# Optimization experiments

Measured on AMD Instinct MI355X. Metric: run time of the kernel, lower is better.

The kernel has to match this reference:

```python
import jax, jax.numpy as jnp
import numpy as np

N_HEADS = 8
N_GROUPS = 32
EPS = 1e-6


def setup_inputs() -> dict:
    key = jax.random.key(0)
    ks = jax.random.split(key, 8)
    b, c, n, K = 2, 512, 1024, 64
    x = jax.random.normal(ks[0], (b, c, n), dtype=jnp.float32)
    valid_mask = jax.random.randint(ks[1], (n, K), 0, 2, dtype=jnp.int32)
    # ensure every query attends to at least one key (avoids all--inf softmax rows)
    valid_mask = valid_mask.at[:, 0].set(1)
    attend_idx = jax.random.randint(ks[2], (n, K), 0, n, dtype=jnp.int64)
    scale = 0.03
    return {
        "x": x,
        "valid_mask": valid_mask,
        "attend_idx": attend_idx,
        "gn_gamma": jnp.ones((c,), jnp.float32),
        "gn_beta": jnp.zeros((c,), jnp.float32),
        "wq": jax.random.normal(ks[3], (c, c), jnp.float32) * scale,
        "bq": jnp.zeros((c,), jnp.float32),
        "wk": jax.random.normal(ks[4], (c, c), jnp.float32) * scale,
        "bk": jnp.zeros((c,), jnp.float32),
        "wv": jax.random.normal(ks[5], (c, c), jnp.float32) * scale,
        "bv": jnp.zeros((c,), jnp.float32),
        "wo": jax.random.normal(ks[6], (c, c), jnp.float32) * scale,
        "bo": jnp.zeros((c,), jnp.float32),
    }


def _group_norm(x, gamma, beta):
    b, c, n = x.shape
    xr = x.reshape(b, N_GROUPS, c // N_GROUPS, n)
    mu = xr.mean(axis=(2, 3), keepdims=True)
    var = xr.var(axis=(2, 3), keepdims=True)
    h = ((xr - mu) * jax.lax.rsqrt(var + EPS)).reshape(b, c, n)
    return h * gamma[None, :, None] + beta[None, :, None]


def reference(x, valid_mask, attend_idx, gn_gamma, gn_beta,
              wq, bq, wk, bk, wv, bv, wo, bo):
    b, c, n = x.shape
    H = N_HEADS
    dh = c // H
    h = _group_norm(x, gn_gamma, gn_beta)
    # 1x1 Conv1d == per-node linear projection
    proj = lambda w, bias: jnp.einsum('oc,bcn->bon', w, h) + bias[None, :, None]
    q = proj(wq, bq).reshape(b, H, dh, n)
    k = proj(wk, bk).reshape(b, H, dh, n)
    v = proj(wv, bv).reshape(b, H, dh, n)
    # gather attendable keys/values per query: [b, H, nq, K, dh]
    kT = jnp.transpose(k, (0, 1, 3, 2))  # [b, H, n, dh]
    vT = jnp.transpose(v, (0, 1, 3, 2))
    keys = jnp.take(kT, attend_idx, axis=2)
    vals = jnp.take(vT, attend_idx, axis=2)
    # NOTE: sparse_forward uses beta=1 (no 1/sqrt(dh) scaling)
    w = jnp.einsum('bhqkc,bhcq->bhqk', keys, q)
    w = jnp.where(valid_mask[None, None] == 0, -jnp.inf, w)
    w = jax.nn.softmax(w, axis=-1)
    o = jnp.einsum('bhqk,bhqkc->bhqc', w, vals)  # [b, H, n, dh]
    # permute(0,3,1,2).reshape(b,c,n): channel layout is (dh, H)
    o = jnp.transpose(o, (0, 3, 1, 2)).reshape(b, c, n)
    out = x + jnp.einsum('oc,bcn->bon', wo, o) + bo[None, :, None]
    return out
```

## Files before the change

### kernel.cpp

```cpp
#include <hip/hip_runtime.h>
#include <hip/hip_bf16.h>

#define B_   2
#define C_   512
#define N_   1024
#define KK_  64
#define H_   8
#define DH_  64
#define NG_  32
#define MQKV 1536

typedef __attribute__((ext_vector_type(8))) short short8;
typedef __attribute__((ext_vector_type(4))) float f32x4;

__device__ __forceinline__ float ldf(const void* p, size_t i, int isbf) {
  return isbf ? __bfloat162float(((const __hip_bfloat16*)p)[i])
              : ((const float*)p)[i];
}
__device__ __forceinline__ unsigned short f2bfu(float f) {
  __hip_bfloat16 h = __float2bfloat16(f);
  unsigned short u; __builtin_memcpy(&u, &h, 2); return u;
}
__device__ __forceinline__ float bfu2f(unsigned short u) {
  return __uint_as_float(((unsigned)u) << 16);
}
__device__ __forceinline__ int detect_bf(const void* gamma) {
  return ((const unsigned*)gamma)[0] == 0x3F803F80u;
}
__device__ __forceinline__ uint4 ld8_bf(const void* w, size_t off, int isbf) {
  if (isbf) return *(const uint4*)((const unsigned short*)w + off);
  float4 a = *(const float4*)((const float*)w + off);
  float4 b = *(const float4*)((const float*)w + off + 4);
  uint4 u;
  u.x = (unsigned)f2bfu(a.x) | ((unsigned)f2bfu(a.y) << 16);
  u.y = (unsigned)f2bfu(a.z) | ((unsigned)f2bfu(a.w) << 16);
  u.z = (unsigned)f2bfu(b.x) | ((unsigned)f2bfu(b.y) << 16);
  u.w = (unsigned)f2bfu(b.z) | ((unsigned)f2bfu(b.w) << 16);
  return u;
}

__global__ __launch_bounds__(256) void conv_k(
    const void* x, const void* wq, const void* wk, const void* wv,
    const void* gamma, unsigned short* __restrict__ wqkvS,
    float2* __restrict__ part) {
  const int isbf = detect_bf(gamma);
  const int tid = threadIdx.x;
  const int idx = blockIdx.x * 256 + tid;
  {
    int m = idx >> 9, c = idx & 511;
    const void* src = (m < 512) ? wq : (m < 1024 ? wk : wv);
    wqkvS[idx] = f2bfu(ldf(src, (size_t)(m & 511) * C_ + c, isbf));
  }

  __shared__ float ssum[256], ssq[256];
  if (blockIdx.x < 256) {
    const size_t base = (size_t)blockIdx.x * 4096;
    float sum = 0.f, sq = 0.f;
    if (isbf) {
      const uint4* p = (const uint4*)((const unsigned short*)x + base);
      for (int t = tid; t < 512; t += 256) {
        uint4 u = p[t];
        unsigned wv4[4] = {u.x, u.y, u.z, u.w};
#pragma unroll
        for (int q = 0; q < 4; q++) {
          float a = __uint_as_float(wv4[q] << 16);
          float b = __uint_as_float(wv4[q] & 0xffff0000u);
          sum += a + b; sq += a * a + b * b;
        }
      }
    } else {
      const float4* p = (const float4*)((const float*)x + base);
      for (int t = tid; t < 1024; t += 256) {
        float4 v = p[t];
        sum += v.x + v.y + v.z + v.w;
        sq  += v.x * v.x + v.y * v.y + v.z * v.z + v.w * v.w;
      }
    }
    ssum[tid] = sum; ssq[tid] = sq;
    __syncthreads();
    for (int s = 128; s > 0; s >>= 1) {
      if (tid < s) { ssum[tid] += ssum[tid + s]; ssq[tid] += ssq[tid + s]; }
      __syncthreads();
    }
    if (tid == 0) part[blockIdx.x] = make_float2(ssum[0], ssq[0]);
  }
}

__global__ __launch_bounds__(256) void gn_apply_k(
    const void* x, const void* gamma, const void* beta,
    const float2* __restrict__ part, unsigned short* __restrict__ hT) {
  const int isbf = detect_bf(gamma);
  const int n0 = blockIdx.x * 64, c0 = blockIdx.y * 64, b = blockIdx.z;
  const int tid = threadIdx.x;
  __shared__ unsigned short Lt[64][72];
#pragma unroll
  for (int p = 0; p < 2; p++) {
    int idx = tid + p * 256;
    int cl = idx >> 3, seg = idx & 7;
    int c = c0 + cl;
    int bgi = (b * NG_ + (c >> 4)) * 4;
    float2 p0 = part[bgi], p1 = part[bgi + 1], p2 = part[bgi + 2], p3 = part[bgi + 3];
    float S = p0.x + p1.x + p2.x + p3.x;
    float Q = p0.y + p1.y + p2.y + p3.y;
    float mu = S * (1.f / 16384.f);
    float rs = rsqrtf(fmaxf(Q * (1.f / 16384.f) - mu * mu, 0.f) + 1e-6f);
    float ga = ldf(gamma, c, isbf), be = ldf(beta, c, isbf);
    size_t srow = ((size_t)b * C_ + c) * N_ + n0 + seg * 8;
    float v[8];
    if (isbf) {
      uint4 u = *(const uint4*)((const unsigned short*)x + srow);
      v[0] = __uint_as_float(u.x << 16); v[1] = __uint_as_float(u.x & 0xffff0000u);
      v[2] = __uint_as_float(u.y << 16); v[3] = __uint_as_float(u.y & 0xffff0000u);
      v[4] = __uint_as_float(u.z << 16); v[5] = __uint_as_float(u.z & 0xffff0000u);
      v[6] = __uint_as_float(u.w << 16); v[7] = __uint_as_float(u.w & 0xffff0000u);
    } else {
      float4 a = *(const float4*)((const float*)x + srow);
      float4 bb = *(const float4*)((const float*)x + srow + 4);
      v[0] = a.x; v[1] = a.y; v[2] = a.z; v[3] = a.w;
      v[4] = bb.x; v[5] = bb.y; v[6] = bb.z; v[7] = bb.w;
    }
#pragma unroll
    for (int e = 0; e < 8; e++)
      Lt[seg * 8 + e][cl] = f2bfu((v[e] - mu) * rs * ga + be);
  }
  __syncthreads();
#pragma unroll
  for (int p = 0; p < 2; p++) {
    int idx = tid + p * 256;
    int nl = idx >> 3, seg = idx & 7;
    uint4 v = *(const uint4*)&Lt[nl][seg * 8];
    *(uint4*)&hT[((size_t)b * N_ + n0 + nl) * C_ + c0 + seg * 8] = v;
  }
}

__global__ __launch_bounds__(256) void qkv_gemm_k(
    const unsigned short* __restrict__ wqkvS, const unsigned short* __restrict__ hT,
    const void* bq, const void* bk, const void* bv, const void* gamma,
    unsigned short* __restrict__ qkv) {
  const int isbf = detect_bf(gamma);
  __shared__ short As[2048], Bs[2048];
  const int tid = threadIdx.x;
  const int lane = tid & 63, wave = tid >> 6;
  const int wm = wave >> 1, wn = wave & 1;
  const int n0 = blockIdx.x * 64;
  const int m0 = blockIdx.y * 64;
  const int b  = blockIdx.z;
  const unsigned short* Bbase = hT + (size_t)b * N_ * C_;
  const void* bsrc = (m0 < 512) ? bq : (m0 < 1024 ? bk : bv);

  f32x4 acc[2][2];
#pragma unroll
  for (int i = 0; i < 2; i++)
#pragma unroll
    for (int j = 0; j < 2; j++) acc[i][j] = (f32x4){0.f, 0.f, 0.f, 0.f};

  const int sub = tid >> 6, l = tid & 63;
  const int r = l & 15, kh = (l >> 4) << 3;
  const size_t arow = (size_t)(m0 + sub * 16 + r) * C_;
  const size_t brow = (size_t)(n0 + sub * 16 + r) * C_;

  for (int k0 = 0; k0 < C_; k0 += 32) {
    __syncthreads();
    *(uint4*)&As[tid * 8] = *(const uint4*)&wqkvS[arow + k0 + kh];
    *(uint4*)&Bs[tid * 8] = *(const uint4*)&Bbase[brow + k0 + kh];
    __syncthreads();
    const short8* Av = (const short8*)As;
    const short8* Bv = (const short8*)Bs;
    short8 af[2], bg[2];
#pragma unroll
    for (int i = 0; i < 2; i++) af[i] = Av[(wm * 2 + i) * 64 + lane];
#pragma unroll
    for (int j = 0; j < 2; j++) bg[j] = Bv[(wn * 2 + j) * 64 + lane];
#pragma unroll
    for (int i = 0; i < 2; i++)
#pragma unroll
      for (int j = 0; j < 2; j++)
        acc[i][j] = __builtin_amdgcn_mfma_f32_16x16x32_bf16(af[i], bg[j], acc[i][j], 0, 0, 0);
  }

  const int mb = m0 + wm * 32;
#pragma unroll
  for (int i = 0; i < 2; i++) {
    int mrow0 = mb + i * 16 + ((lane >> 4) << 2);
    int mat = mrow0 >> 9, head = (mrow0 >> 6) & 7, d0 = mrow0 & 63;
    int br = mrow0 & 511;
    float b0 = ldf(bsrc, br, isbf),     b1 = ldf(bsrc, br + 1, isbf);
    float b2 = ldf(bsrc, br + 2, isbf), b3 = ldf(bsrc, br + 3, isbf);
#pragma unroll
    for (int j = 0; j < 2; j++) {
      int n = n0 + wn * 32 + j * 16 + (lane & 15);
      uint2 st;
      st.x = (unsigned)f2bfu(acc[i][j][0] + b0) | ((unsigned)f2bfu(acc[i][j][1] + b1) << 16);
      st.y = (unsigned)f2bfu(acc[i][j][2] + b2) | ((unsigned)f2bfu(acc[i][j][3] + b3) << 16);
      size_t dst = (size_t)mat * ((size_t)B_ * H_ * N_ * DH_) +
                   (((size_t)b * H_ + head) * N_ + n) * DH_ + d0;
      *(uint2*)&qkv[dst] = st;
    }
  }
}

__global__ __launch_bounds__(512) void attn_k(
    const unsigned short* __restrict__ qkv, const void* aidx,
    const int* __restrict__ vmask, unsigned short* __restrict__ ocT) {
  const int tid = threadIdx.x, w = tid >> 6, lane = tid & 63;
  const int b = blockIdx.x >> 10, qi = blockIdx.x & 1023;

  const unsigned* aw = (const unsigned*)aidx;
  unsigned long long bal = __ballot(aw[2 * lane + 1] != 0u);
  const int is64 = (bal == 0ull);

  __shared__ float qs[8][64];
  __shared__ float wl[8][64];
  __shared__ int   il[8][64];
  __shared__ unsigned short olds[512];

  const size_t S = (size_t)B_ * H_ * N_ * DH_;
  const unsigned short* qT = qkv;
  const unsigned short* kT = qkv + S;
  const unsigned short* vT = qkv + 2 * S;
  const size_t bh = ((size_t)b * H_ + w) * N_;

  qs[w][lane] = bfu2f(qT[(bh + qi) * DH_ + lane]);
  const size_t ai = (size_t)qi * KK_ + lane;
  int idx = is64 ? (int)((const long long*)aidx)[ai] : ((const int*)aidx)[ai];
  idx &= (N_ - 1);
  const int valid = vmask[ai];
  __threadfence_block();

  const uint4* k4 = (const uint4*)&kT[(bh + idx) * DH_];
  float s = 0.f;
#pragma unroll
  for (int j2 = 0; j2 < 8; j2++) {
    uint4 u = k4[j2];
    const float* q8 = &qs[w][j2 * 8];
    s += __uint_as_float(u.x << 16) * q8[0] + __uint_as_float(u.x & 0xffff0000u) * q8[1]
       + __uint_as_float(u.y << 16) * q8[2] + __uint_as_float(u.y & 0xffff0000u) * q8[3]
       + __uint_as_float(u.z << 16) * q8[4] + __uint_as_float(u.z & 0xffff0000u) * q8[5]
       + __uint_as_float(u.w << 16) * q8[6] + __uint_as_float(u.w & 0xffff0000u) * q8[7];
  }
  s = valid ? s : -INFINITY;

  float m = s;
#pragma unroll
  for (int off = 32; off > 0; off >>= 1) m = fmaxf(m, __shfl_xor(m, off));
  float e = valid ? __expf(s - m) : 0.f;
  float sum = e;
#pragma unroll
  for (int off = 32; off > 0; off >>= 1) sum += __shfl_xor(sum, off);

  wl[w][lane] = (sum > 0.f) ? (e / sum) : 0.f;
  il[w][lane] = idx;
  __threadfence_block();

  const unsigned short* vbase = vT + bh * DH_;
  float acc = 0.f;
#pragma unroll 16
  for (int ki = 0; ki < KK_; ki++)
    acc += wl[w][ki] * bfu2f(vbase[(size_t)il[w][ki] * DH_ + lane]);

  olds[lane * H_ + w] = f2bfu(acc);
  __syncthreads();
  if (tid < 64) {
    uint4 vv = *(const uint4*)&olds[tid * 8];
    *(uint4*)&ocT[((size_t)b * N_ + qi) * C_ + tid * 8] = vv;
  }
}

__global__ __launch_bounds__(256) void out_gemm_k(
    const void* wo, const unsigned short* __restrict__ ocT,
    const void* bo, const void* __restrict__ x,
    const void* gamma, void* __restrict__ out) {
  const int isbf = detect_bf(gamma);
  __shared__ short As[2048], Bs[2048];
  const int tid = threadIdx.x;
  const int lane = tid & 63, wave = tid >> 6;
  const int wm = wave >> 1, wn = wave & 1;
  const int n0 = blockIdx.x * 64;
  const int m0 = blockIdx.y * 64;
  const int b  = blockIdx.z;
  const unsigned short* Bbase = ocT + (size_t)b * N_ * C_;

  f32x4 acc[2][2];
#pragma unroll
  for (int i = 0; i < 2; i++)
#pragma unroll
    for (int j = 0; j < 2; j++) acc[i][j] = (f32x4){0.f, 0.f, 0.f, 0.f};

  const int sub = tid >> 6, l = tid & 63;
  const int r = l & 15, kh = (l >> 4) << 3;
  const size_t arow = (size_t)(m0 + sub * 16 + r) * C_;
  const size_t brow = (size_t)(n0 + sub * 16 + r) * C_;

  for (int k0 = 0; k0 < C_; k0 += 32) {
    __syncthreads();
    *(uint4*)&As[tid * 8] = ld8_bf(wo, arow + k0 + kh, isbf);
    *(uint4*)&Bs[tid * 8] = *(const uint4*)&Bbase[brow + k0 + kh];
    __syncthreads();
    const short8* Av = (const short8*)As;
    const short8* Bv = (const short8*)Bs;
    short8 af[2], bg[2];
#pragma unroll
    for (int i = 0; i < 2; i++) af[i] = Av[(wm * 2 + i) * 64 + lane];
#pragma unroll
    for (int j = 0; j < 2; j++) bg[j] = Bv[(wn * 2 + j) * 64 + lane];
#pragma unroll
    for (int i = 0; i < 2; i++)
#pragma unroll
      for (int j = 0; j < 2; j++)
        acc[i][j] = __builtin_amdgcn_mfma_f32_16x16x32_bf16(bg[j], af[i], acc[i][j], 0, 0, 0);
  }

#pragma unroll
  for (int i = 0; i < 2; i++) {
    int m = m0 + wm * 32 + i * 16 + (lane & 15);
    float bias = ldf(bo, m, isbf);
#pragma unroll
    for (int j = 0; j < 2; j++) {
      int nb = n0 + wn * 32 + j * 16 + ((lane >> 4) << 2);
      size_t oi = ((size_t)b * C_ + m) * N_ + nb;
      if (isbf) {
        const unsigned short* xp = (const unsigned short*)x;
        uint2 xv = *(const uint2*)&xp[oi];
        uint2 st;
        st.x = (unsigned)f2bfu(bfu2f((unsigned short)(xv.x & 0xffff)) + acc[i][j][0] + bias) |
               ((unsigned)f2bfu(bfu2f((unsigned short)(xv.x >> 16)) + acc[i][j][1] + bias) << 16);
        st.y = (unsigned)f2bfu(bfu2f((unsigned short)(xv.y & 0xffff)) + acc[i][j][2] + bias) |
               ((unsigned)f2bfu(bfu2f((unsigned short)(xv.y >> 16)) + acc[i][j][3] + bias) << 16);
        *(uint2*)&((unsigned short*)out)[oi] = st;
      } else {
        const float* xp = (const float*)x;
        float4 xv = *(const float4*)&xp[oi];
        float4 st;
        st.x = xv.x + acc[i][j][0] + bias;
        st.y = xv.y + acc[i][j][1] + bias;
        st.z = xv.z + acc[i][j][2] + bias;
        st.w = xv.w + acc[i][j][3] + bias;
        *(float4*)&((float*)out)[oi] = st;
      }
    }
  }
}

extern "C" void kernel_launch(void* const* d_in, const int* in_sizes, int n_in,
                              void* d_out, int out_size, void* d_ws, size_t ws_size,
                              hipStream_t stream) {
  const void* x     = d_in[0];
  const int*  vmask = (const int*)d_in[1];
  const void* aidx  = d_in[2];
  const void* gamma = d_in[3];
  const void* beta  = d_in[4];
  const void* wq = d_in[5],  *bq = d_in[6];
  const void* wk = d_in[7],  *bk = d_in[8];
  const void* wv = d_in[9],  *bv = d_in[10];
  const void* wo = d_in[11], *bo = d_in[12];

  unsigned short* qkv = (unsigned short*)d_ws;
  unsigned short* hT  = qkv + (size_t)3 * B_ * H_ * N_ * DH_;
  unsigned short* ocT = hT;
  unsigned short* wqkvS = (unsigned short*)d_out;
  float2* part = (float2*)((char*)d_out + (size_t)MQKV * C_ * 2);

  conv_k<<<(MQKV * C_) / 256, 256, 0, stream>>>(x, wq, wk, wv, gamma, wqkvS, part);
  gn_apply_k<<<dim3(N_ / 64, C_ / 64, B_), 256, 0, stream>>>(x, gamma, beta, part, hT);
  qkv_gemm_k<<<dim3(N_ / 64, MQKV / 64, B_), 256, 0, stream>>>(
      wqkvS, hT, bq, bk, bv, gamma, qkv);
  attn_k<<<B_ * N_, 512, 0, stream>>>(qkv, aidx, vmask, ocT);
  out_gemm_k<<<dim3(N_ / 64, C_ / 64, B_), 256, 0, stream>>>(wo, ocT, bo, x, gamma, d_out);
}
```

Baseline: 147.7 us.

## Double-buffer GEMM tiles via global_load_lds DMA, pre-convert wo, pair-vectorize attention V gather

Both GEMMs now stage 64-wide K chunks into double-buffered LDS with direct global-to-LDS loads, prefetching the next chunk while MFMAs run on the current one. This halves the number of barrier pairs and hides load latency. The output projection weight is converted to bf16 once in conv_k when the workspace is large enough, so the GEMM can DMA it directly. The attention value accumulation splits keys across the two half-waves and loads two bf16 values per lane, then reduces them with a shuffle. This costs more LDS per block and relies on the workspace size check.

```diff
diff --git a/kernel.cpp b/kernel.cpp
--- a/kernel.cpp
+++ b/kernel.cpp
@@ -38,11 +38,16 @@
   u.w = (unsigned)f2bfu(b.z) | ((unsigned)f2bfu(b.w) << 16);
   return u;
 }
+__device__ __forceinline__ void dma16(const void* g, void* l) {
+  __builtin_amdgcn_global_load_lds(
+      (const __attribute__((address_space(1))) unsigned*)g,
+      (__attribute__((address_space(3))) unsigned*)l, 16, 0, 0);
+}
 
 __global__ __launch_bounds__(256) void conv_k(
-    const void* x, const void* wq, const void* wk, const void* wv,
+    const void* x, const void* wq, const void* wk, const void* wv, const void* wo,
     const void* gamma, unsigned short* __restrict__ wqkvS,
-    float2* __restrict__ part) {
+    unsigned short* __restrict__ woS, float2* __restrict__ part) {
   const int isbf = detect_bf(gamma);
   const int tid = threadIdx.x;
   const int idx = blockIdx.x * 256 + tid;
@@ -50,6 +55,10 @@
     int m = idx >> 9, c = idx & 511;
     const void* src = (m < 512) ? wq : (m < 1024 ? wk : wv);
     wqkvS[idx] = f2bfu(ldf(src, (size_t)(m & 511) * C_ + c, isbf));
+  }
+  if (woS != nullptr && blockIdx.x >= 1024 && blockIdx.x < 2048) {
+    int i2 = (blockIdx.x - 1024) * 256 + tid;
+    woS[i2] = f2bfu(ldf(wo, i2, isbf));
   }
 
   __shared__ float ssum[256], ssq[256];
@@ -138,7 +147,7 @@
     const void* bq, const void* bk, const void* bv, const void* gamma,
     unsigned short* __restrict__ qkv) {
   const int isbf = detect_bf(gamma);
-  __shared__ short As[2048], Bs[2048];
+  __shared__ short As[8192], Bs[8192];
   const int tid = threadIdx.x;
   const int lane = tid & 63, wave = tid >> 6;
   const int wm = wave >> 1, wn = wave & 1;
@@ -148,35 +157,48 @@
   const unsigned short* Bbase = hT + (size_t)b * N_ * C_;
   const void* bsrc = (m0 < 512) ? bq : (m0 < 1024 ? bk : bv);
 
+  const int r = lane & 15, kh = (lane >> 4) << 3;
+  const size_t arow = (size_t)(m0 + wave * 16 + r) * C_;
+  const size_t brow = (size_t)(n0 + wave * 16 + r) * C_;
+  short* Ad = &As[wave * 512];
+  short* Bd = &Bs[wave * 512];
+
   f32x4 acc[2][2];
 #pragma unroll
   for (int i = 0; i < 2; i++)
 #pragma unroll
     for (int j = 0; j < 2; j++) acc[i][j] = (f32x4){0.f, 0.f, 0.f, 0.f};
 
-  const int sub = tid >> 6, l = tid & 63;
-  const int r = l & 15, kh = (l >> 4) << 3;
-  const size_t arow = (size_t)(m0 + sub * 16 + r) * C_;
-  const size_t brow = (size_t)(n0 + sub * 16 + r) * C_;
-
-  for (int k0 = 0; k0 < C_; k0 += 32) {
+#define STAGE_Q(bufv, k0v)                                              \
+  { dma16(&wqkvS[arow + (k0v) + kh],      Ad + (bufv) * 4096);          \
+    dma16(&wqkvS[arow + (k0v) + 32 + kh], Ad + (bufv) * 4096 + 2048);   \
+    dma16(&Bbase[brow + (k0v) + kh],      Bd + (bufv) * 4096);          \
+    dma16(&Bbase[brow + (k0v) + 32 + kh], Bd + (bufv) * 4096 + 2048); }
+
+  STAGE_Q(0, 0);
+  __syncthreads();
+  int buf = 0;
+  for (int t = 0; t < 8; ++t) {
+    if (t < 7) STAGE_Q(buf ^ 1, (t + 1) * 64);
+#pragma unroll
+    for (int s = 0; s < 2; ++s) {
+      const short8* Av = (const short8*)&As[buf * 4096 + s * 2048];
+      const short8* Bv = (const short8*)&Bs[buf * 4096 + s * 2048];
+      short8 af[2], bg[2];
+#pragma unroll
+      for (int i = 0; i < 2; i++) af[i] = Av[(wm * 2 + i) * 64 + lane];
+#pragma unroll
+      for (int j = 0; j < 2; j++) bg[j] = Bv[(wn * 2 + j) * 64 + lane];
+#pragma unroll
+      for (int i = 0; i < 2; i++)
+#pragma unroll
+        for (int j = 0; j < 2; j++)
+          acc[i][j] = __builtin_amdgcn_mfma_f32_16x16x32_bf16(af[i], bg[j], acc[i][j], 0, 0, 0);
+    }
     __syncthreads();
-    *(uint4*)&As[tid * 8] = *(const uint4*)&wqkvS[arow + k0 + kh];
-    *(uint4*)&Bs[tid * 8] = *(const uint4*)&Bbase[brow + k0 + kh];
-    __syncthreads();
-    const short8* Av = (const short8*)As;
-    const short8* Bv = (const short8*)Bs;
-    short8 af[2], bg[2];
-#pragma unroll
-    for (int i = 0; i < 2; i++) af[i] = Av[(wm * 2 + i) * 64 + lane];
-#pragma unroll
-    for (int j = 0; j < 2; j++) bg[j] = Bv[(wn * 2 + j) * 64 + lane];
-#pragma unroll
-    for (int i = 0; i < 2; i++)
-#pragma unroll
-      for (int j = 0; j < 2; j++)
-        acc[i][j] = __builtin_amdgcn_mfma_f32_16x16x32_bf16(af[i], bg[j], acc[i][j], 0, 0, 0);
-  }
+    buf ^= 1;
+  }
+#undef STAGE_Q
 
   const int mb = m0 + wm * 32;
 #pragma unroll
@@ -253,12 +275,22 @@
   __threadfence_block();
 
   const unsigned short* vbase = vT + bh * DH_;
-  float acc = 0.f;
-#pragma unroll 16
-  for (int ki = 0; ki < KK_; ki++)
-    acc += wl[w][ki] * bfu2f(vbase[(size_t)il[w][ki] * DH_ + lane]);
-
-  olds[lane * H_ + w] = f2bfu(acc);
+  const int half = lane >> 5, dhp = lane & 31;
+  float a0 = 0.f, a1 = 0.f;
+#pragma unroll 8
+  for (int ki = 0; ki < KK_ / 2; ki++) {
+    int key = 2 * ki + half;
+    float wgt = wl[w][key];
+    unsigned uv = *(const unsigned*)&vbase[(size_t)il[w][key] * DH_ + 2 * dhp];
+    a0 += wgt * __uint_as_float(uv << 16);
+    a1 += wgt * __uint_as_float(uv & 0xffff0000u);
+  }
+  a0 += __shfl_xor(a0, 32);
+  a1 += __shfl_xor(a1, 32);
+  if (half == 0) {
+    olds[(2 * dhp) * H_ + w]     = f2bfu(a0);
+    olds[(2 * dhp + 1) * H_ + w] = f2bfu(a1);
+  }
   __syncthreads();
   if (tid < 64) {
     uint4 vv = *(const uint4*)&olds[tid * 8];
@@ -267,11 +299,12 @@
 }
 
 __global__ __launch_bounds__(256) void out_gemm_k(
-    const void* wo, const unsigned short* __restrict__ ocT,
+    const void* wo, const unsigned short* __restrict__ woS,
+    const unsigned short* __restrict__ ocT,
     const void* bo, const void* __restrict__ x,
     const void* gamma, void* __restrict__ out) {
   const int isbf = detect_bf(gamma);
-  __shared__ short As[2048], Bs[2048];
+  __shared__ short As[8192], Bs[8192];
   const int tid = threadIdx.x;
   const int lane = tid & 63, wave = tid >> 6;
   const int wm = wave >> 1, wn = wave & 1;
@@ -279,6 +312,13 @@
   const int m0 = blockIdx.y * 64;
   const int b  = blockIdx.z;
   const unsigned short* Bbase = ocT + (size_t)b * N_ * C_;
+  const unsigned short* asrc = woS ? woS : (isbf ? (const unsigned short*)wo : nullptr);
+
+  const int r = lane & 15, kh = (lane >> 4) << 3;
+  const size_t arow = (size_t)(m0 + wave * 16 + r) * C_;
+  const size_t brow = (size_t)(n0 + wave * 16 + r) * C_;
+  short* Ad = &As[wave * 512];
+  short* Bd = &Bs[wave * 512];
 
   f32x4 acc[2][2];
 #pragma unroll
@@ -286,29 +326,41 @@
 #pragma unroll
     for (int j = 0; j < 2; j++) acc[i][j] = (f32x4){0.f, 0.f, 0.f, 0.f};
 
-  const int sub = tid >> 6, l = tid & 63;
-  const int r = l & 15, kh = (l >> 4) << 3;
-  const size_t arow = (size_t)(m0 + sub * 16 + r) * C_;
-  const size_t brow = (size_t)(n0 + sub * 16 + r) * C_;
-
-  for (int k0 = 0; k0 < C_; k0 += 32) {
+#define STAGE_O(bufv, k0v)                                                        \
+  { if (asrc) {                                                                   \
+      dma16(&asrc[arow + (k0v) + kh],      Ad + (bufv) * 4096);                   \
+      dma16(&asrc[arow + (k0v) + 32 + kh], Ad + (bufv) * 4096 + 2048);            \
+    } else {                                                                      \
+      *(uint4*)&As[(bufv) * 4096 + tid * 8]        = ld8_bf(wo, arow + (k0v) + kh, 0);      \
+      *(uint4*)&As[(bufv) * 4096 + 2048 + tid * 8] = ld8_bf(wo, arow + (k0v) + 32 + kh, 0); \
+    }                                                                             \
+    dma16(&Bbase[brow + (k0v) + kh],      Bd + (bufv) * 4096);                    \
+    dma16(&Bbase[brow + (k0v) + 32 + kh], Bd + (bufv) * 4096 + 2048); }
+
+  STAGE_O(0, 0);
+  __syncthreads();
+  int buf = 0;
+  for (int t = 0; t < 8; ++t) {
+    if (t < 7) STAGE_O(buf ^ 1, (t + 1) * 64);
+#pragma unroll
+    for (int s = 0; s < 2; ++s) {
+      const short8* Av = (const short8*)&As[buf * 4096 + s * 2048];
+      const short8* Bv = (const short8*)&Bs[buf * 4096 + s * 2048];
+      short8 af[2], bg[2];
+#pragma unroll
+      for (int i = 0; i < 2; i++) af[i] = Av[(wm * 2 + i) * 64 + lane];
+#pragma unroll
+      for (int j = 0; j < 2; j++) bg[j] = Bv[(wn * 2 + j) * 64 + lane];
+#pragma unroll
+      for (int i = 0; i < 2; i++)
+#pragma unroll
+        for (int j = 0; j < 2; j++)
+          acc[i][j] = __builtin_amdgcn_mfma_f32_16x16x32_bf16(bg[j], af[i], acc[i][j], 0, 0, 0);
+    }
     __syncthreads();
-    *(uint4*)&As[tid * 8] = ld8_bf(wo, arow + k0 + kh, isbf);
-    *(uint4*)&Bs[tid * 8] = *(const uint4*)&Bbase[brow + k0 + kh];
-    __syncthreads();
-    const short8* Av = (const short8*)As;
-    const short8* Bv = (const short8*)Bs;
-    short8 af[2], bg[2];
-#pragma unroll
-    for (int i = 0; i < 2; i++) af[i] = Av[(wm * 2 + i) * 64 + lane];
-#pragma unroll
-    for (int j = 0; j < 2; j++) bg[j] = Bv[(wn * 2 + j) * 64 + lane];
-#pragma unroll
-    for (int i = 0; i < 2; i++)
-#pragma unroll
-      for (int j = 0; j < 2; j++)
-        acc[i][j] = __builtin_amdgcn_mfma_f32_16x16x32_bf16(bg[j], af[i], acc[i][j], 0, 0, 0);
-  }
+    buf ^= 1;
+  }
+#undef STAGE_O
 
 #pragma unroll
   for (int i = 0; i < 2; i++) {
@@ -359,11 +411,16 @@
   unsigned short* ocT = hT;
   unsigned short* wqkvS = (unsigned short*)d_out;
   float2* part = (float2*)((char*)d_out + (size_t)MQKV * C_ * 2);
-
-  conv_k<<<(MQKV * C_) / 256, 256, 0, stream>>>(x, wq, wk, wv, gamma, wqkvS, part);
+  unsigned short* woS = nullptr;
+  if (ws_size >= ((size_t)8 << 20) + (size_t)C_ * C_ * 2)
+    woS = (unsigned short*)((char*)d_ws + ((size_t)8 << 20));
+
+  conv_k<<<(MQKV * C_) / 256, 256, 0, stream>>>(x, wq, wk, wv, wo, gamma,
+                                                wqkvS, woS, part);
   gn_apply_k<<<dim3(N_ / 64, C_ / 64, B_), 256, 0, stream>>>(x, gamma, beta, part, hT);
   qkv_gemm_k<<<dim3(N_ / 64, MQKV / 64, B_), 256, 0, stream>>>(
       wqkvS, hT, bq, bk, bv, gamma, qkv);
   attn_k<<<B_ * N_, 512, 0, stream>>>(qkv, aidx, vmask, ocT);
-  out_gemm_k<<<dim3(N_ / 64, C_ / 64, B_), 256, 0, stream>>>(wo, ocT, bo, x, gamma, d_out);
-}
+  out_gemm_k<<<dim3(N_ / 64, C_ / 64, B_), 256, 0, stream>>>(
+      wo, woS, ocT, bo, x, gamma, d_out);
+}
```

Measured after the change: 139.9 us. 5.3% less time.
